# Optimization experiments

Measured on AMD Instinct MI355X. Metric: run time of the kernel, lower is better.

## Reference

```python
import jax, jax.numpy as jnp
import numpy as np

B, C, H, W = 4, 256, 64, 64
D = C // 8  # qk projection dim = 32


def setup_inputs() -> dict:
    key = jax.random.key(0)
    ks = jax.random.split(key, 10)
    s = 1.0 / np.sqrt(C)
    return {
        "semantic_map": jax.random.normal(ks[0], (B, C, H, W), jnp.float32),
        "structural_map": jax.random.normal(ks[1], (B, C, H, W), jnp.float32),
        "Wq": jax.random.normal(ks[2], (D, C), jnp.float32) * s,
        "bq": jax.random.normal(ks[3], (D,), jnp.float32) * 0.01,
        "Wk": jax.random.normal(ks[4], (D, C), jnp.float32) * s,
        "bk": jax.random.normal(ks[5], (D,), jnp.float32) * 0.01,
        "Wv": jax.random.normal(ks[6], (C, C), jnp.float32) * s,
        "bv": jax.random.normal(ks[7], (C,), jnp.float32) * 0.01,
        "gamma": jnp.zeros((1,), jnp.float32) + 0.5,  # nonzero so the attention path matters
    }


def reference(semantic_map, structural_map, Wq, bq, Wk, bk, Wv, bv, gamma):
    b, c, h, w = semantic_map.shape
    n = h * w
    # 1x1 convs == per-pixel linear projections
    q = jnp.einsum("bchw,dc->bdhw", semantic_map, Wq) + bq[None, :, None, None]
    k = jnp.einsum("bchw,dc->bdhw", structural_map, Wk) + bk[None, :, None, None]
    v = jnp.einsum("bchw,oc->bohw", structural_map, Wv) + bv[None, :, None, None]
    q = q.reshape(b, -1, n).transpose(0, 2, 1)  # (B, HW, D)
    k = k.reshape(b, -1, n)                     # (B, D, HW)
    v = v.reshape(b, c, n)                      # (B, C, HW)
    energy = jnp.einsum("bid,bdj->bij", q, k)   # (B, HW, HW)
    attention = jax.nn.softmax(energy, axis=-1)
    # out[b,c,i] = sum_j v[b,c,j] * attention[b,i,j]
    out = jnp.einsum("bcj,bij->bci", v, attention).reshape(b, c, h, w)
    return gamma * out + semantic_map
```

## Files before the change

kernel.cpp:

```cpp
#include <hip/hip_runtime.h>

#define B_   4
#define C_   256
#define N_   4096
#define D_   32
#define CP   264

typedef _Float16 half8  __attribute__((ext_vector_type(8)));
typedef _Float16 half4v __attribute__((ext_vector_type(4)));
typedef _Float16 half2v __attribute__((ext_vector_type(2)));
typedef float    f32x4  __attribute__((ext_vector_type(4)));

__global__ __launch_bounds__(256) void wcvt_kernel(
    const float* __restrict__ Wq, const float* __restrict__ Wk,
    const float* __restrict__ Wv, _Float16* __restrict__ Wh)
{
    const int idx = blockIdx.x * 256 + threadIdx.x;
    const int kk  = idx & 31;
    const int row = (idx >> 5) & 15;
    const int kc  = (idx >> 9) & 7;
    const int t   = idx >> 12;
    const int c   = kc*32 + kk;
    float v;
    if (t < 2)      v = Wq[(t*16 + row)*C_ + c];
    else if (t < 4) v = Wk[((t-2)*16 + row)*C_ + c];
    else            v = Wv[((t-4)*16 + row)*C_ + c];
    Wh[idx] = (_Float16)v;
}

__global__ __launch_bounds__(512, 2) void proj_kernel(
    const float* __restrict__ sem, const float* __restrict__ str,
    const _Float16* __restrict__ Wh,
    const float* __restrict__ bq, const float* __restrict__ bk,
    const float* __restrict__ bv,
    _Float16* __restrict__ Qh, _Float16* __restrict__ Kh, _Float16* __restrict__ Vh2)
{
    __shared__ __align__(16) _Float16 s_x[64 * CP];
    __shared__ __align__(16) _Float16 s_s[64 * CP];
    __shared__ __align__(16) _Float16 s_v[8][3][1024];

    const int bid = blockIdx.x;
    const int nt6 = bid & 63;
    const int b   = bid >> 6;
    const int n0  = nt6 * 64;
    const int tid = threadIdx.x;
    const int w    = tid >> 6;
    const int lane = tid & 63;
    const int quad = lane >> 4;
    const int l15  = lane & 15;

    const int cnt = (w < 4) ? 3 : 2;
    const int t0  = (w < 4) ? w*3 : 12 + (w-4)*2;

    f32x4 acc[3][4];
    #pragma unroll
    for (int i = 0; i < 3; ++i)
        #pragma unroll
        for (int j = 0; j < 4; ++j) { acc[i][j][0]=0.f; acc[i][j][1]=0.f; acc[i][j][2]=0.f; acc[i][j][3]=0.f; }

    const size_t xbase = (size_t)b * C_ * N_;

    #pragma unroll
    for (int r = 0; r < 4; ++r) {
        const int slot = r*512 + tid;
        const int nq = slot & 15;
        const int cp = slot >> 4;
        const float* p0 = str + xbase + (size_t)(2*cp) * N_ + n0 + nq*4;
        const float4 a4 = *(const float4*)p0;
        const float4 b4 = *(const float4*)(p0 + N_);
        #pragma unroll
        for (int t = 0; t < 4; ++t) {
            half2v hp; hp[0] = (_Float16)a4[t]; hp[1] = (_Float16)b4[t];
            *(half2v*)(s_x + (nq*4 + t)*CP + 2*cp) = hp;
        }
        const float* p1 = sem + xbase + (size_t)(2*cp) * N_ + n0 + nq*4;
        const float4 c4 = *(const float4*)p1;
        const float4 d4 = *(const float4*)(p1 + N_);
        #pragma unroll
        for (int t = 0; t < 4; ++t) {
            half2v hp; hp[0] = (_Float16)c4[t]; hp[1] = (_Float16)d4[t];
            *(half2v*)(s_s + (nq*4 + t)*CP + 2*cp) = hp;
        }
    }
    __syncthreads();

    auto afload = [&](half8 (&af)[3], int kc) {
        #pragma unroll
        for (int mi = 0; mi < 3; ++mi)
            if (mi < cnt)
                af[mi] = *(const half8*)(Wh + ((size_t)(((t0+mi)*8 + kc)*16 + l15))*32 + quad*8);
    };
    auto bload = [&](half8 (&bfr)[4], half8 (&sfr)[4], int kc) {
        #pragma unroll
        for (int nt = 0; nt < 4; ++nt)
            bfr[nt] = *(const half8*)(s_x + (nt*16 + l15)*CP + kc*32 + quad*8);
        if (w == 0) {
            #pragma unroll
            for (int nt = 0; nt < 4; ++nt)
                sfr[nt] = *(const half8*)(s_s + (nt*16 + l15)*CP + kc*32 + quad*8);
        }
    };
    auto domfma = [&](const half8 (&af)[3], const half8 (&bfr)[4], const half8 (&sfr)[4]) {
        #pragma unroll
        for (int mi = 0; mi < 3; ++mi) {
            if (mi >= cnt) break;
            const bool useS = (t0 + mi) < 2;
            #pragma unroll
            for (int nt = 0; nt < 4; ++nt)
                acc[mi][nt] = __builtin_amdgcn_mfma_f32_16x16x32_f16(
                                  af[mi], useS ? sfr[nt] : bfr[nt], acc[mi][nt], 0, 0, 0);
        }
    };

    half8 afA[3], afB[3];
    afload(afA, 0);
    #pragma unroll 1
    for (int kc2 = 0; kc2 < 4; ++kc2) {
        const int kc = kc2*2;
        half8 bfr[4], sfr[4];
        bload(bfr, sfr, kc);
        afload(afB, kc+1);
        domfma(afA, bfr, sfr);
        half8 bfr2[4], sfr2[4];
        bload(bfr2, sfr2, kc+1);
        if (kc2 < 3) afload(afA, kc+2);
        domfma(afB, bfr2, sfr2);
    }

    #pragma unroll
    for (int mi = 0; mi < 3; ++mi) {
        if (mi >= cnt) break;
        const int t = t0 + mi;
        if (t < 4) {
            const bool isq = (t < 2);
            const int  tt  = isq ? t : (t - 2);
            f32x4 b4 = *(const f32x4*)((isq ? bq : bk) + tt*16 + quad*4);
            _Float16* dst = isq ? Qh : Kh;
            const int dc  = tt*2 + (quad >> 1);
            const int off = (quad & 1) * 4;
            #pragma unroll
            for (int nt = 0; nt < 4; ++nt) {
                const int n = n0 + nt*16 + l15;
                f32x4 a = acc[mi][nt];
                half4v hq;
                hq[0]=(_Float16)(a[0]+b4[0]); hq[1]=(_Float16)(a[1]+b4[1]);
                hq[2]=(_Float16)(a[2]+b4[2]); hq[3]=(_Float16)(a[3]+b4[3]);
                *(half4v*)(dst + ((size_t)(b*4 + dc) * N_ + n) * 8 + off) = hq;
            }
        } else {
            const int ctg = t - 4;
            f32x4 b4 = *(const f32x4*)(bv + ctg*16 + quad*4);
            #pragma unroll
            for (int nt = 0; nt < 4; ++nt) {
                const int js = nt & 1;
                const int hb = nt >> 1;
                f32x4 a = acc[mi][nt];
                #pragma unroll
                for (int r = 0; r < 4; ++r)
                    s_v[w][mi][hb*512 + ((l15>>2)*16 + quad*4 + r)*8 + js*4 + (l15&3)]
                        = (_Float16)(a[r] + b4[r]);
            }
        }
    }
    {
        _Float16* vb = Vh2 + (size_t)b * (size_t)N_ * C_;
        const int jc2_0 = n0 >> 5;
        #pragma unroll
        for (int mi = 0; mi < 3; ++mi) {
            if (mi >= cnt) break;
            const int t = t0 + mi;
            if (t >= 4) {
                const int ctg = t - 4;
                #pragma unroll
                for (int hb = 0; hb < 2; ++hb) {
                    half8 vv = *(const half8*)(&s_v[w][mi][hb*512 + lane*8]);
                    *(half8*)(vb + (size_t)(jc2_0 + hb)*8192 + (size_t)ctg*512 + lane*8) = vv;
                }
            }
        }
    }
}

__global__ __launch_bounds__(512, 2) void flash_kernel(
    const _Float16* __restrict__ Qh, const _Float16* __restrict__ Kh,
    const _Float16* __restrict__ Vh2, const float* __restrict__ sem,
    const float* __restrict__ gma, float* __restrict__ out)
{
    __shared__ float s_mp[8*64];
    __shared__ float s_lp[8*64];
    __shared__ __align__(16) float s_red[8][64][32];

    const int g   = blockIdx.x;
    const int xcd = g & 7;
    const int b   = xcd >> 1;
    const int i0  = ((xcd & 1)*32 + (g >> 3)) * 64;
    const int tid = threadIdx.x;
    const int w    = tid >> 6;
    const int lane = tid & 63;
    const int quad = lane >> 4;
    const int l15  = lane & 15;
    const int wc   = w >> 1;
    const int wj   = w & 1;

    const _Float16* qk_base = Qh + (size_t)(b*4 + quad) * N_ * 8;
    half8 qf[4];
    #pragma unroll
    for (int i = 0; i < 4; ++i)
        qf[i] = *(const half8*)(qk_base + (size_t)(i0 + i*16 + l15) * 8);

    const _Float16* klane = Kh + ((size_t)(b*4 + quad) * N_ + l15) * 8;
    const _Float16* vl    = Vh2 + (size_t)b * (size_t)N_ * C_
                            + (size_t)(wc*4) * 512 + (size_t)lane * 8;

    float mx[4];
    #pragma unroll
    for (int i = 0; i < 4; ++i) mx[i] = -3e38f;
    {
        half8 kp[4], kn[4];
        auto kl4 = [&](half8 (&kf)[4], int j0) {
            #pragma unroll
            for (int js = 0; js < 4; ++js)
                kf[js] = *(const half8*)(klane + (size_t)(j0 + js*16) * 8);
        };
        auto p0step = [&](const half8 (&kf)[4], half8 (&kfn)[4], int j0, bool more) {
            if (more) kl4(kfn, j0 + 64);
            #pragma unroll
            for (int js = 0; js < 4; ++js) {
                f32x4 z; z[0]=0.f; z[1]=0.f; z[2]=0.f; z[3]=0.f;
                #pragma unroll
                for (int i = 0; i < 4; ++i) {
                    f32x4 s = __builtin_amdgcn_mfma_f32_16x16x32_f16(kf[js], qf[i], z, 0, 0, 0);
                    #pragma unroll
                    for (int r = 0; r < 4; ++r) mx[i] = fmaxf(mx[i], s[r]);
                }
            }
        };
        kl4(kp, w*512);
        #pragma unroll 1
        for (int it2 = 0; it2 < 4; ++it2) {
            const int j0 = w*512 + it2*128;
            p0step(kp, kn, j0, true);
            p0step(kn, kp, j0 + 64, it2 < 3);
        }
    }
    #pragma unroll
    for (int i = 0; i < 4; ++i) {
        mx[i] = fmaxf(mx[i], __shfl_xor(mx[i], 16));
        mx[i] = fmaxf(mx[i], __shfl_xor(mx[i], 32));
    }
    {
        const float mv = (lane < 16) ? mx[0] : (lane < 32) ? mx[1] : (lane < 48) ? mx[2] : mx[3];
        s_mp[w*64 + lane] = mv;
    }
    __syncthreads();
    float mf[4];
    #pragma unroll
    for (int i = 0; i < 4; ++i) {
        float m = -3e38f;
        #pragma unroll
        for (int ww = 0; ww < 8; ++ww) m = fmaxf(m, s_mp[ww*64 + i*16 + l15]);
        mf[i] = m;
    }

    f32x4 acc[4][4];
    #pragma unroll
    for (int ct = 0; ct < 4; ++ct)
        #pragma unroll
        for (int i = 0; i < 4; ++i) { acc[ct][i][0]=0.f; acc[ct][i][1]=0.f; acc[ct][i][2]=0.f; acc[ct][i][3]=0.f; }
    float l4[4] = {0.f, 0.f, 0.f, 0.f};

    half8 kA[2], kB[2], vA[4], vB[4];

    auto kl2 = [&](half8 (&kf)[2], int j0) {
        kf[0] = *(const half8*)(klane + (size_t)j0 * 8);
        kf[1] = *(const half8*)(klane + (size_t)(j0 + 16) * 8);
    };
    auto vl4 = [&](half8 (&vf)[4], int j0) {
        const _Float16* p = vl + (size_t)(j0 >> 5) * 8192;
        #pragma unroll
        for (int ct = 0; ct < 4; ++ct)
            vf[ct] = *(const half8*)(p + ct*512);
    };
    auto mkp = [](const f32x4& s, float mfv, float& lacc) -> half4v {
        float e0 = __expf(s[0]-mfv), e1 = __expf(s[1]-mfv);
        float e2 = __expf(s[2]-mfv), e3 = __expf(s[3]-mfv);
        lacc += (e0+e1)+(e2+e3);
        half2v p01 = __builtin_bit_cast(half2v, __builtin_amdgcn_cvt_pkrtz(e0, e1));
        half2v p23 = __builtin_bit_cast(half2v, __builtin_amdgcn_cvt_pkrtz(e2, e3));
        return __builtin_shufflevector(p01, p23, 0, 1, 2, 3);
    };

    auto step = [&](const half8 (&kf)[2], const half8 (&vf)[4],
                    half8 (&kfn)[2], half8 (&vfn)[4], int j0, bool more) {
        f32x4 z; z[0]=0.f; z[1]=0.f; z[2]=0.f; z[3]=0.f;
        f32x4 sf0[4], sf1[4];
        #pragma unroll
        for (int i = 0; i < 4; ++i)
            sf0[i] = __builtin_amdgcn_mfma_f32_16x16x32_f16(kf[0], qf[i], z, 0, 0, 0);
        #pragma unroll
        for (int i = 0; i < 4; ++i)
            sf1[i] = __builtin_amdgcn_mfma_f32_16x16x32_f16(kf[1], qf[i], z, 0, 0, 0);
        if (more) {
            kl2(kfn, j0 + 32);
            vl4(vfn, j0 + 32);
        }
        half8 pcat[4];
        #pragma unroll
        for (int i = 0; i < 4; ++i) {
            half4v pa = mkp(sf0[i], mf[i], l4[i]);
            half4v pb = mkp(sf1[i], mf[i], l4[i]);
            pcat[i] = __builtin_shufflevector(pa, pb, 0, 1, 2, 3, 4, 5, 6, 7);
        }
        __builtin_amdgcn_s_setprio(1);
        #pragma unroll
        for (int ct = 0; ct < 4; ++ct)
            #pragma unroll
            for (int i = 0; i < 4; ++i)
                acc[ct][i] = __builtin_amdgcn_mfma_f32_16x16x32_f16(vf[ct], pcat[i], acc[ct][i], 0, 0, 0);
        __builtin_amdgcn_s_setprio(0);
    };

    const int jb = wj * 2048;
    kl2(kA, jb);
    vl4(vA, jb);
    #pragma unroll 1
    for (int s2 = 0; s2 < 32; ++s2) {
        const int j0 = jb + s2*64;
        step(kA, vA, kB, vB, j0, true);
        step(kB, vB, kA, vA, j0 + 32, s2 < 31);
    }

    #pragma unroll
    for (int i = 0; i < 4; ++i) {
        l4[i] += __shfl_xor(l4[i], 16);
        l4[i] += __shfl_xor(l4[i], 32);
    }
    {
        const float lv = (lane < 16) ? l4[0] : (lane < 32) ? l4[1] : (lane < 48) ? l4[2] : l4[3];
        s_lp[w*64 + lane] = lv;
    }

    const int kx = (lane & 7) << 2;
    const int cput = wj ? 0 : 2;
    #pragma unroll
    for (int t2 = 0; t2 < 2; ++t2)
        #pragma unroll
        for (int i = 0; i < 4; ++i)
            *(f32x4*)&s_red[w][lane][(t2*16 + i*4) ^ kx] = acc[cput + t2][i];
    __syncthreads();

    float sc[4];
    {
        const float gv = gma[0];
        #pragma unroll
        for (int i = 0; i < 4; ++i) {
            const float lt = s_lp[(w & ~1)*64 + 64*0 + i*16 + l15]
                           + s_lp[((w & ~1) | 1)*64 + i*16 + l15];
            sc[i] = gv / lt;
        }
    }
    const int cown = wj ? 2 : 0;
    #pragma unroll
    for (int t2 = 0; t2 < 2; ++t2) {
        #pragma unroll
        for (int i = 0; i < 4; ++i) {
            f32x4 r = acc[cown + t2][i];
            f32x4 o = *(const f32x4*)&s_red[w ^ 1][lane][(t2*16 + i*4) ^ kx];
            r[0]+=o[0]; r[1]+=o[1]; r[2]+=o[2]; r[3]+=o[3];
            const int c0 = (wc*4 + cown + t2)*16 + quad*4;
            #pragma unroll
            for (int r4 = 0; r4 < 4; ++r4) {
                const size_t idx = ((size_t)(b*C_ + c0 + r4)) * N_ + i0 + i*16 + l15;
                out[idx] = r[r4] * sc[i] + sem[idx];
            }
        }
    }
}

extern "C" void kernel_launch(void* const* d_in, const int* in_sizes, int n_in,
                              void* d_out, int out_size, void* d_ws, size_t ws_size,
                              hipStream_t stream) {
    const float* sem = (const float*)d_in[0];
    const float* str = (const float*)d_in[1];
    const float* Wq  = (const float*)d_in[2];
    const float* bq  = (const float*)d_in[3];
    const float* Wk  = (const float*)d_in[4];
    const float* bk  = (const float*)d_in[5];
    const float* Wv  = (const float*)d_in[6];
    const float* bv  = (const float*)d_in[7];
    const float* gma = (const float*)d_in[8];
    float* out = (float*)d_out;

    _Float16* Qh  = (_Float16*)d_ws;
    _Float16* Kh  = Qh + (size_t)B_*N_*D_;
    _Float16* Vh2 = Kh + (size_t)B_*N_*D_;
    _Float16* Wh  = Vh2 + (size_t)B_*C_*N_;

    hipLaunchKernelGGL(wcvt_kernel, dim3(320), dim3(256), 0, stream, Wq, Wk, Wv, Wh);
    hipLaunchKernelGGL(proj_kernel, dim3(B_*(N_/64)), dim3(512), 0, stream,
                       sem, str, Wh, bq, bk, bv, Qh, Kh, Vh2);
    hipLaunchKernelGGL(flash_kernel, dim3(256), dim3(512), 0, stream,
                       Qh, Kh, Vh2, sem, gma, out);
}
```

Baseline: 177.1 us.

## Stage K/V tiles through double-buffered LDS shared across waves in flash kernel

The flash kernel's work split changes. Before, each wave loaded its own K/V fragments from global memory and handled half the key range, with a cross-wave reduction at the end. Now each wave owns a 16-row query slice and a half of the channels over the full key range. The block cooperatively stages 64-key K and V tiles into double-buffered shared memory, with a barrier per tile. This removes redundant global V loads and the final s_red reduction, at the cost of per-iteration syncs and LDS read traffic. The projection kernel also reuses its input staging buffer for the V transpose to cut shared memory usage.

After: 175.4 us. Within noise of the previous version (-1.0%).

```diff
diff --git a/kernel.cpp b/kernel.cpp
--- a/kernel.cpp
+++ b/kernel.cpp
@@ -10,6 +10,7 @@
 typedef _Float16 half4v __attribute__((ext_vector_type(4)));
 typedef _Float16 half2v __attribute__((ext_vector_type(2)));
 typedef float    f32x4  __attribute__((ext_vector_type(4)));
+typedef int      i32x4  __attribute__((ext_vector_type(4)));
 
 __global__ __launch_bounds__(256) void wcvt_kernel(
     const float* __restrict__ Wq, const float* __restrict__ Wk,
@@ -35,9 +36,9 @@
     const float* __restrict__ bv,
     _Float16* __restrict__ Qh, _Float16* __restrict__ Kh, _Float16* __restrict__ Vh2)
 {
-    __shared__ __align__(16) _Float16 s_x[64 * CP];
-    __shared__ __align__(16) _Float16 s_s[64 * CP];
-    __shared__ __align__(16) _Float16 s_v[8][3][1024];
+    __shared__ __align__(16) _Float16 smem[2 * 64 * CP];
+    _Float16* s_x = smem;
+    _Float16* s_s = smem + 64 * CP;
 
     const int bid = blockIdx.x;
     const int nt6 = bid & 63;
@@ -147,9 +148,18 @@
                 hq[2]=(_Float16)(a[2]+b4[2]); hq[3]=(_Float16)(a[3]+b4[3]);
                 *(half4v*)(dst + ((size_t)(b*4 + dc) * N_ + n) * 8 + off) = hq;
             }
-        } else {
+        }
+    }
+    __syncthreads();
+
+    #pragma unroll
+    for (int mi = 0; mi < 3; ++mi) {
+        if (mi >= cnt) break;
+        const int t = t0 + mi;
+        if (t >= 4) {
             const int ctg = t - 4;
             f32x4 b4 = *(const f32x4*)(bv + ctg*16 + quad*4);
+            _Float16* sv = smem + (w*3 + mi)*1024;
             #pragma unroll
             for (int nt = 0; nt < 4; ++nt) {
                 const int js = nt & 1;
@@ -157,7 +167,7 @@
                 f32x4 a = acc[mi][nt];
                 #pragma unroll
                 for (int r = 0; r < 4; ++r)
-                    s_v[w][mi][hb*512 + ((l15>>2)*16 + quad*4 + r)*8 + js*4 + (l15&3)]
+                    sv[hb*512 + ((l15>>2)*16 + quad*4 + r)*8 + js*4 + (l15&3)]
                         = (_Float16)(a[r] + b4[r]);
             }
         }
@@ -171,9 +181,10 @@
             const int t = t0 + mi;
             if (t >= 4) {
                 const int ctg = t - 4;
+                const _Float16* sv = smem + (w*3 + mi)*1024;
                 #pragma unroll
                 for (int hb = 0; hb < 2; ++hb) {
-                    half8 vv = *(const half8*)(&s_v[w][mi][hb*512 + lane*8]);
+                    half8 vv = *(const half8*)(&sv[hb*512 + lane*8]);
                     *(half8*)(vb + (size_t)(jc2_0 + hb)*8192 + (size_t)ctg*512 + lane*8) = vv;
                 }
             }
@@ -186,31 +197,29 @@
     const _Float16* __restrict__ Vh2, const float* __restrict__ sem,
     const float* __restrict__ gma, float* __restrict__ out)
 {
+    __shared__ __align__(16) _Float16 sK[2][4*64*8];
+    __shared__ __align__(16) _Float16 sV[2][2*8192];
     __shared__ float s_mp[8*64];
-    __shared__ float s_lp[8*64];
-    __shared__ __align__(16) float s_red[8][64][32];
-
-    const int g   = blockIdx.x;
-    const int xcd = g & 7;
+
+    const int bid = blockIdx.x;
+    const int xcd = bid & 7;
     const int b   = xcd >> 1;
-    const int i0  = ((xcd & 1)*32 + (g >> 3)) * 64;
+    const int i0  = ((xcd & 1)*32 + (bid >> 3)) * 64;
     const int tid = threadIdx.x;
     const int w    = tid >> 6;
     const int lane = tid & 63;
     const int quad = lane >> 4;
     const int l15  = lane & 15;
-    const int wc   = w >> 1;
-    const int wj   = w & 1;
+    const int wif  = w >> 1;
+    const int wc   = w & 1;
 
     const _Float16* qk_base = Qh + (size_t)(b*4 + quad) * N_ * 8;
-    half8 qf[4];
+    half8 qfs[4];
     #pragma unroll
     for (int i = 0; i < 4; ++i)
-        qf[i] = *(const half8*)(qk_base + (size_t)(i0 + i*16 + l15) * 8);
+        qfs[i] = *(const half8*)(qk_base + (size_t)(i0 + i*16 + l15) * 8);
 
     const _Float16* klane = Kh + ((size_t)(b*4 + quad) * N_ + l15) * 8;
-    const _Float16* vl    = Vh2 + (size_t)b * (size_t)N_ * C_
-                            + (size_t)(wc*4) * 512 + (size_t)lane * 8;
 
     float mx[4];
     #pragma unroll
@@ -229,7 +238,7 @@
                 f32x4 z; z[0]=0.f; z[1]=0.f; z[2]=0.f; z[3]=0.f;
                 #pragma unroll
                 for (int i = 0; i < 4; ++i) {
-                    f32x4 s = __builtin_amdgcn_mfma_f32_16x16x32_f16(kf[js], qf[i], z, 0, 0, 0);
+                    f32x4 s = __builtin_amdgcn_mfma_f32_16x16x32_f16(kf[js], qfs[i], z, 0, 0, 0);
                     #pragma unroll
                     for (int r = 0; r < 4; ++r) mx[i] = fmaxf(mx[i], s[r]);
                 }
@@ -249,37 +258,42 @@
         mx[i] = fmaxf(mx[i], __shfl_xor(mx[i], 32));
     }
     {
-        const float mv = (lane < 16) ? mx[0] : (lane < 32) ? mx[1] : (lane < 48) ? mx[2] : mx[3];
+        const float mv = (quad == 0) ? mx[0] : (quad == 1) ? mx[1] : (quad == 2) ? mx[2] : mx[3];
         s_mp[w*64 + lane] = mv;
     }
     __syncthreads();
-    float mf[4];
-    #pragma unroll
-    for (int i = 0; i < 4; ++i) {
-        float m = -3e38f;
-        #pragma unroll
-        for (int ww = 0; ww < 8; ++ww) m = fmaxf(m, s_mp[ww*64 + i*16 + l15]);
-        mf[i] = m;
-    }
-
-    f32x4 acc[4][4];
-    #pragma unroll
-    for (int ct = 0; ct < 4; ++ct)
-        #pragma unroll
-        for (int i = 0; i < 4; ++i) { acc[ct][i][0]=0.f; acc[ct][i][1]=0.f; acc[ct][i][2]=0.f; acc[ct][i][3]=0.f; }
-    float l4[4] = {0.f, 0.f, 0.f, 0.f};
-
-    half8 kA[2], kB[2], vA[4], vB[4];
-
-    auto kl2 = [&](half8 (&kf)[2], int j0) {
-        kf[0] = *(const half8*)(klane + (size_t)j0 * 8);
-        kf[1] = *(const half8*)(klane + (size_t)(j0 + 16) * 8);
-    };
-    auto vl4 = [&](half8 (&vf)[4], int j0) {
-        const _Float16* p = vl + (size_t)(j0 >> 5) * 8192;
-        #pragma unroll
-        for (int ct = 0; ct < 4; ++ct)
-            vf[ct] = *(const half8*)(p + ct*512);
+    float mf = -3e38f;
+    #pragma unroll
+    for (int ww = 0; ww < 8; ++ww)
+        mf = fmaxf(mf, s_mp[ww*64 + wif*16 + l15]);
+
+    const half8 qf = (wif == 0) ? qfs[0] : (wif == 1) ? qfs[1] : (wif == 2) ? qfs[2] : qfs[3];
+
+    f32x4 acc[8];
+    #pragma unroll
+    for (int ct = 0; ct < 8; ++ct) { acc[ct][0]=0.f; acc[ct][1]=0.f; acc[ct][2]=0.f; acc[ct][3]=0.f; }
+    float lsum = 0.f;
+
+    const _Float16* vbB = Vh2 + (size_t)b * (size_t)N_ * C_;
+    const int kq  = tid >> 6;
+    const int kjj = tid & 63;
+
+    i32x4 vr[4]; i32x4 kr;
+    auto stage_issue = [&](int j0) {
+        const i32x4* vsrc = (const i32x4*)(vbB + (size_t)(j0 >> 5) * 8192);
+        #pragma unroll
+        for (int r = 0; r < 4; ++r)
+            vr[r] = vsrc[r*512 + tid];
+        if (tid < 256)
+            kr = *(const i32x4*)(Kh + ((size_t)(b*4 + kq) * N_ + j0 + kjj) * 8);
+    };
+    auto stage_write = [&](int s) {
+        i32x4* vd = (i32x4*)sV[s];
+        #pragma unroll
+        for (int r = 0; r < 4; ++r)
+            vd[r*512 + tid] = vr[r];
+        if (tid < 256)
+            ((i32x4*)sK[s])[tid] = kr;
     };
     auto mkp = [](const f32x4& s, float mfv, float& lacc) -> half4v {
         float e0 = __expf(s[0]-mfv), e1 = __expf(s[1]-mfv);
@@ -290,89 +304,58 @@
         return __builtin_shufflevector(p01, p23, 0, 1, 2, 3);
     };
 
-    auto step = [&](const half8 (&kf)[2], const half8 (&vf)[4],
-                    half8 (&kfn)[2], half8 (&vfn)[4], int j0, bool more) {
+    stage_issue(0);
+    stage_write(0);
+    __syncthreads();
+
+    #pragma unroll 1
+    for (int t = 0; t < 64; ++t) {
+        const int cur = t & 1;
+        if (t < 63) stage_issue((t + 1) * 64);
+
+        half8 kf[4];
+        #pragma unroll
+        for (int js = 0; js < 4; ++js)
+            kf[js] = *(const half8*)(sK[cur] + (quad*64 + js*16 + l15) * 8);
         f32x4 z; z[0]=0.f; z[1]=0.f; z[2]=0.f; z[3]=0.f;
-        f32x4 sf0[4], sf1[4];
-        #pragma unroll
-        for (int i = 0; i < 4; ++i)
-            sf0[i] = __builtin_amdgcn_mfma_f32_16x16x32_f16(kf[0], qf[i], z, 0, 0, 0);
-        #pragma unroll
-        for (int i = 0; i < 4; ++i)
-            sf1[i] = __builtin_amdgcn_mfma_f32_16x16x32_f16(kf[1], qf[i], z, 0, 0, 0);
-        if (more) {
-            kl2(kfn, j0 + 32);
-            vl4(vfn, j0 + 32);
-        }
-        half8 pcat[4];
-        #pragma unroll
-        for (int i = 0; i < 4; ++i) {
-            half4v pa = mkp(sf0[i], mf[i], l4[i]);
-            half4v pb = mkp(sf1[i], mf[i], l4[i]);
-            pcat[i] = __builtin_shufflevector(pa, pb, 0, 1, 2, 3, 4, 5, 6, 7);
-        }
+        f32x4 sf[4];
+        #pragma unroll
+        for (int js = 0; js < 4; ++js)
+            sf[js] = __builtin_amdgcn_mfma_f32_16x16x32_f16(kf[js], qf, z, 0, 0, 0);
+
+        half4v p0 = mkp(sf[0], mf, lsum);
+        half4v p1 = mkp(sf[1], mf, lsum);
+        half4v p2 = mkp(sf[2], mf, lsum);
+        half4v p3 = mkp(sf[3], mf, lsum);
+        half8 pc0 = __builtin_shufflevector(p0, p1, 0, 1, 2, 3, 4, 5, 6, 7);
+        half8 pc1 = __builtin_shufflevector(p2, p3, 0, 1, 2, 3, 4, 5, 6, 7);
+
+        const _Float16* vbase = sV[cur] + (wc*8)*512 + lane*8;
         __builtin_amdgcn_s_setprio(1);
         #pragma unroll
-        for (int ct = 0; ct < 4; ++ct)
-            #pragma unroll
-            for (int i = 0; i < 4; ++i)
-                acc[ct][i] = __builtin_amdgcn_mfma_f32_16x16x32_f16(vf[ct], pcat[i], acc[ct][i], 0, 0, 0);
+        for (int ct = 0; ct < 8; ++ct) {
+            half8 v0 = *(const half8*)(vbase + ct*512);
+            half8 v1 = *(const half8*)(vbase + 8192 + ct*512);
+            acc[ct] = __builtin_amdgcn_mfma_f32_16x16x32_f16(v0, pc0, acc[ct], 0, 0, 0);
+            acc[ct] = __builtin_amdgcn_mfma_f32_16x16x32_f16(v1, pc1, acc[ct], 0, 0, 0);
+        }
         __builtin_amdgcn_s_setprio(0);
-    };
-
-    const int jb = wj * 2048;
-    kl2(kA, jb);
-    vl4(vA, jb);
-    #pragma unroll 1
-    for (int s2 = 0; s2 < 32; ++s2) {
-        const int j0 = jb + s2*64;
-        step(kA, vA, kB, vB, j0, true);
-        step(kB, vB, kA, vA, j0 + 32, s2 < 31);
-    }
-
-    #pragma unroll
-    for (int i = 0; i < 4; ++i) {
-        l4[i] += __shfl_xor(l4[i], 16);
-        l4[i] += __shfl_xor(l4[i], 32);
-    }
-    {
-        const float lv = (lane < 16) ? l4[0] : (lane < 32) ? l4[1] : (lane < 48) ? l4[2] : l4[3];
-        s_lp[w*64 + lane] = lv;
-    }
-
-    const int kx = (lane & 7) << 2;
-    const int cput = wj ? 0 : 2;
-    #pragma unroll
-    for (int t2 = 0; t2 < 2; ++t2)
-        #pragma unroll
-        for (int i = 0; i < 4; ++i)
-            *(f32x4*)&s_red[w][lane][(t2*16 + i*4) ^ kx] = acc[cput + t2][i];
-    __syncthreads();
-
-    float sc[4];
-    {
-        const float gv = gma[0];
-        #pragma unroll
-        for (int i = 0; i < 4; ++i) {
-            const float lt = s_lp[(w & ~1)*64 + 64*0 + i*16 + l15]
-                           + s_lp[((w & ~1) | 1)*64 + i*16 + l15];
-            sc[i] = gv / lt;
-        }
-    }
-    const int cown = wj ? 2 : 0;
-    #pragma unroll
-    for (int t2 = 0; t2 < 2; ++t2) {
-        #pragma unroll
-        for (int i = 0; i < 4; ++i) {
-            f32x4 r = acc[cown + t2][i];
-            f32x4 o = *(const f32x4*)&s_red[w ^ 1][lane][(t2*16 + i*4) ^ kx];
-            r[0]+=o[0]; r[1]+=o[1]; r[2]+=o[2]; r[3]+=o[3];
-            const int c0 = (wc*4 + cown + t2)*16 + quad*4;
-            #pragma unroll
-            for (int r4 = 0; r4 < 4; ++r4) {
-                const size_t idx = ((size_t)(b*C_ + c0 + r4)) * N_ + i0 + i*16 + l15;
-                out[idx] = r[r4] * sc[i] + sem[idx];
-            }
+
+        if (t < 63) stage_write(cur ^ 1);
+        __syncthreads();
+    }
+
+    lsum += __shfl_xor(lsum, 16);
+    lsum += __shfl_xor(lsum, 32);
+    const float sc = gma[0] / lsum;
+    const int irow = i0 + wif*16 + l15;
+    #pragma unroll
+    for (int ct = 0; ct < 8; ++ct) {
+        const int c0 = (wc*8 + ct)*16 + quad*4;
+        #pragma unroll
+        for (int r4 = 0; r4 < 4; ++r4) {
+            const size_t idx = ((size_t)(b*C_ + c0 + r4)) * N_ + irow;
+            out[idx] = acc[ct][r4] * sc + sem[idx];
         }
     }
 }
```
